# Performance work log

Measured on AMD Instinct MI355X. Metric: run time of the kernel, lower is better.

The kernel has to match this reference:

```python
import jax, jax.numpy as jnp
import numpy as np

B, S, D, H = 4, 2048, 1024, 16
NEG = -1e10  # matches the module's -10000000000.0 additive mask


def setup_inputs() -> dict:
    key = jax.random.key(0)
    k1, k2, k3, k4, k5 = jax.random.split(key, 5)
    scale = 0.02
    return {
        "x": jax.random.normal(k1, (B, S, D), dtype=jnp.float32),
        "w_qkv": jax.random.normal(k2, (D, 3 * D), dtype=jnp.float32) * scale,
        "b_qkv": jax.random.normal(k3, (3 * D,), dtype=jnp.float32) * scale,
        "w_out": jax.random.normal(k4, (D, D), dtype=jnp.float32) * scale,
        "b_out": jax.random.normal(k5, (D,), dtype=jnp.float32) * scale,
    }


def reference(x, w_qkv, b_qkv, w_out, b_out):
    b, s, d = x.shape
    hd = d // H  # per-head dim
    qkv = x @ w_qkv + b_qkv  # [b,s,3d]
    qq, kk, vv = jnp.split(qkv, 3, axis=-1)
    # [b,h,s,hd]
    qq = qq.reshape(b, s, H, hd).transpose(0, 2, 1, 3)
    kk = kk.reshape(b, s, H, hd).transpose(0, 2, 1, 3)
    vv = vv.reshape(b, s, H, hd).transpose(0, 2, 1, 3)
    scale = 1.0 / float(hd) ** 0.5
    # additive causal mask: NEG above diagonal, 0 on/below (as in module)
    mask = (1.0 - jnp.tri(s, dtype=jnp.float32)) * NEG
    attn = jnp.einsum("bhqd,bhkd->bhqk", qq, kk) * scale + mask
    attn = jax.nn.softmax(attn, axis=-1)
    out = jnp.einsum("bhqk,bhkd->bhqd", attn, vv)  # [b,h,s,hd]
    out = out.transpose(0, 2, 1, 3).reshape(b, s, d)
    return out @ w_out + b_out
```

## Files before the change

### kernel.cpp

```cpp
#include <hip/hip_runtime.h>
#include <hip/hip_bf16.h>
#include <stdint.h>


#define B_   4
#define S_   2048
#define D_   1024
#define H_   16
#define HD_  64
#define MTOK (B_ * S_)
#define BK   32
#define QSCALE 0.18033688011112042f

typedef __attribute__((ext_vector_type(8))) short bfx8;
typedef __attribute__((ext_vector_type(4))) float fx4;

static __device__ __forceinline__ unsigned short f2bf(float f) {
    union { float f; uint32_t u; } v{f};
    uint32_t u = v.u;
    u += 0x7fffu + ((u >> 16) & 1u);
    return (unsigned short)(u >> 16);
}

static __device__ __forceinline__ uint32_t cvtpk(float lo, float hi) {
    uint32_t r;
    asm volatile("v_cvt_pk_bf16_f32 %0, %1, %2" : "=v"(r) : "v"(lo), "v"(hi));
    return r;
}

static __device__ __forceinline__ void gll16(const unsigned short* g, const unsigned short* l) {
    typedef const __attribute__((address_space(1))) void* gp_t;
    typedef __attribute__((address_space(3))) void* lp_t;
    __builtin_amdgcn_global_load_lds((gp_t)(uintptr_t)g, (lp_t)(uint32_t)(uintptr_t)l, 16, 0, 0);
}

__global__ void k_conv_x(const float* __restrict__ x, unsigned short* __restrict__ xb, int n8) {
    int i = blockIdx.x * blockDim.x + threadIdx.x;
    int stride = gridDim.x * blockDim.x;
    for (; i < n8; i += stride) {
        const float4* p = (const float4*)(x + (size_t)i * 8);
        float4 a = p[0], b = p[1];
        bfx8 o;
        o[0]=f2bf(a.x); o[1]=f2bf(a.y); o[2]=f2bf(a.z); o[3]=f2bf(a.w);
        o[4]=f2bf(b.x); o[5]=f2bf(b.y); o[6]=f2bf(b.z); o[7]=f2bf(b.w);
        *(bfx8*)(xb + (size_t)i * 8) = o;
    }
}

__global__ void k_transpose_bf(const float* __restrict__ w, unsigned short* __restrict__ wt,
                               int K, int N) {
    int idx = blockIdx.x * blockDim.x + threadIdx.x;
    int total = N * (K / 8);
    if (idx >= total) return;
    int n  = idx % N;
    int k0 = (idx / N) * 8;
    bfx8 o;
#pragma unroll
    for (int j = 0; j < 8; ++j) o[j] = f2bf(w[(size_t)(k0 + j) * N + n]);
    *(bfx8*)(wt + (size_t)n * K + k0) = o;
}

__global__ void k_transpose_v(const unsigned short* __restrict__ Vw,
                              unsigned short* __restrict__ Vt) {
    __shared__ unsigned short lds[64][72];
    const int bg = blockIdx.x;
    const int bh = bg >> 5;
    const int st = (bg & 31) * 64;
    const int t = threadIdx.x;
#pragma unroll
    for (int j = 0; j < 2; ++j) {
        int c = t + 256 * j;
        int row = c >> 3, q = c & 7;
        *(bfx8*)&lds[row][q * 8] = *(const bfx8*)&Vw[((size_t)bh * S_ + st + row) * HD_ + q * 8];
    }
    __syncthreads();
#pragma unroll
    for (int j = 0; j < 2; ++j) {
        int c = t + 256 * j;
        int d = c >> 3, q = c & 7;
        bfx8 o;
#pragma unroll
        for (int e = 0; e < 8; ++e) o[e] = lds[q * 8 + e][d];
        *(bfx8*)&Vt[((size_t)bh * HD_ + d) * S_ + st + q * 8] = o;
    }
}

__launch_bounds__(256)
__global__ void k_gemm_qkv(const unsigned short* __restrict__ A,
                           const unsigned short* __restrict__ Bt,
                           const float* __restrict__ bias,
                           unsigned short* __restrict__ Qw,
                           unsigned short* __restrict__ Kw,
                           unsigned short* __restrict__ Vw) {
    __shared__ unsigned short Al[128 * BK];
    __shared__ unsigned short Bl[128 * BK];
    const int wg = blockIdx.x;
    const int lin = (wg & 7) * 192 + (wg >> 3);
    const int ny = lin / 24, nx = lin - ny * 24;
    const int m0 = ny * 128;
    const int n0 = nx * 128;
    const int t = threadIdx.x;
    const int w = t >> 6, l = t & 63;
    const int wr = w >> 1, wc = w & 1;
    const int lr = l & 15, lg = l >> 4;
    const int srow = l >> 2;
    const int scol = (l & 3) * 8;
    fx4 acc[4][4] = {};

    for (int k0 = 0; k0 < D_; k0 += BK) {
        __syncthreads();
#pragma unroll
        for (int j = 0; j < 2; ++j) {
            int rb = j * 64 + w * 16;
            gll16(&A [(size_t)(m0 + rb + srow) * D_ + k0 + scol], &Al[rb * BK]);
            gll16(&Bt[(size_t)(n0 + rb + srow) * D_ + k0 + scol], &Bl[rb * BK]);
        }
        __syncthreads();
        bfx8 af[4], bf[4];
#pragma unroll
        for (int i = 0; i < 4; ++i) af[i] = *(const bfx8*)&Al[(wr * 64 + i * 16 + lr) * BK + lg * 8];
#pragma unroll
        for (int i = 0; i < 4; ++i) bf[i] = *(const bfx8*)&Bl[(wc * 64 + i * 16 + lr) * BK + lg * 8];
#pragma unroll
        for (int mi = 0; mi < 4; ++mi)
#pragma unroll
            for (int ni = 0; ni < 4; ++ni)
                acc[mi][ni] = __builtin_amdgcn_mfma_f32_16x16x32_bf16(bf[ni], af[mi], acc[mi][ni], 0, 0, 0);
    }

#pragma unroll
    for (int ni = 0; ni < 4; ++ni) {
        const int nn = n0 + wc * 64 + ni * 16 + lg * 4;
        const int mat = nn >> 10;
        const int h = (nn & 1023) >> 6, dd = nn & 63;
        const float4 bv = *(const float4*)&bias[nn];
        unsigned short* dst = (mat == 0) ? Qw : (mat == 1) ? Kw : Vw;
        const float sc = (mat == 0) ? QSCALE : 1.0f;
#pragma unroll
        for (int mi = 0; mi < 4; ++mi) {
            const int m = m0 + wr * 64 + mi * 16 + lr;
            const int b = m >> 11, s = m & 2047;
            const int bh = b * H_ + h;
            fx4 v = acc[mi][ni];
            float o0 = (v[0] + bv.x) * sc, o1 = (v[1] + bv.y) * sc;
            float o2 = (v[2] + bv.z) * sc, o3 = (v[3] + bv.w) * sc;
            uint2 u; u.x = cvtpk(o0, o1); u.y = cvtpk(o2, o3);
            *(uint2*)&dst[((size_t)bh * S_ + s) * HD_ + dd] = u;
        }
    }
}

__launch_bounds__(512, 4)
__global__ void k_attn(const unsigned short* __restrict__ Qw,
                       const unsigned short* __restrict__ Kw,
                       const unsigned short* __restrict__ Vt,
                       unsigned short* __restrict__ Ob) {
    __shared__ unsigned short Kl[2][64 * 64];
    __shared__ unsigned short Vl[2][64 * 64];
    __shared__ unsigned short Pl[8][16 * 72];
    const int wg = blockIdx.x;
    const int xcd = wg & 7, ix = wg >> 3;
    const int bh = xcd * 8 + (ix >> 3);
    const int pi = ix & 7;
    const int t = threadIdx.x;
    const int w = t >> 6, l = t & 63;
    const int lr = l & 15, lg = l >> 4;
    const int qA = pi * 128 + w * 16;
    const int qB = (15 - pi) * 128 + w * 16;
    const int NT = 32 - 2 * pi;

    const unsigned short* Qp = Qw + (size_t)bh * S_ * HD_;
    const unsigned short* Kp = Kw + (size_t)bh * S_ * HD_;
    const unsigned short* Vp = Vt + (size_t)bh * HD_ * S_;

    bfx8 qfA[2], qfB[2];
#pragma unroll
    for (int kk = 0; kk < 2; ++kk) {
        qfA[kk] = *(const bfx8*)&Qp[(size_t)(qA + lr) * HD_ + kk * 32 + lg * 8];
        qfB[kk] = *(const bfx8*)&Qp[(size_t)(qB + lr) * HD_ + kk * 32 + lg * 8];
    }

    fx4 oA[4] = {}, oB[4] = {};
    float mA = -1e30f, lA = 0.f, mB = -1e30f, lB = 0.f;

    auto compute = [&](int qr, const bfx8* qf, fx4* oacc, float& mrow, float& lsum,
                       int kv0, int buf) {
        fx4 sacc[4] = {};
#pragma unroll
        for (int c = 0; c < 4; ++c) {
            int row = c * 16 + lr;
#pragma unroll
            for (int kk = 0; kk < 2; ++kk) {
                int colb = kk * 64 + lg * 16;
                bfx8 kf = *(const bfx8*)((const char*)&Kl[buf][0] + row * 128 + (colb ^ ((row & 7) << 4)));
                sacc[c] = __builtin_amdgcn_mfma_f32_16x16x32_bf16(kf, qf[kk], sacc[c], 0, 0, 0);
            }
        }
        if (kv0 + 63 > qr) {
            const int qrel = qr + lr - kv0;
#pragma unroll
            for (int c = 0; c < 4; ++c)
#pragma unroll
                for (int i = 0; i < 4; ++i)
                    if (c * 16 + lg * 4 + i > qrel) sacc[c][i] = -1e30f;
        }
        float mc0 = fmaxf(fmaxf(sacc[0][0], sacc[0][1]), fmaxf(sacc[0][2], sacc[0][3]));
        float mc1 = fmaxf(fmaxf(sacc[1][0], sacc[1][1]), fmaxf(sacc[1][2], sacc[1][3]));
        float mc2 = fmaxf(fmaxf(sacc[2][0], sacc[2][1]), fmaxf(sacc[2][2], sacc[2][3]));
        float mc3 = fmaxf(fmaxf(sacc[3][0], sacc[3][1]), fmaxf(sacc[3][2], sacc[3][3]));
        float mx = fmaxf(fmaxf(mc0, mc1), fmaxf(mc2, mc3));
        mx = fmaxf(mx, __shfl_xor(mx, 16));
        mx = fmaxf(mx, __shfl_xor(mx, 32));
        float mnew = fmaxf(mrow, mx);
        float al = exp2f(mrow - mnew);
        mrow = mnew;
        float ps = 0.f;
        uint32_t pk[4][2];
#pragma unroll
        for (int c = 0; c < 4; ++c)
#pragma unroll
            for (int r = 0; r < 2; ++r) {
                float p0 = exp2f(sacc[c][2 * r]     - mnew);
                float p1 = exp2f(sacc[c][2 * r + 1] - mnew);
                ps += p0 + p1;
                pk[c][r] = cvtpk(p0, p1);
            }
        ps += __shfl_xor(ps, 16);
        ps += __shfl_xor(ps, 32);
        lsum = lsum * al + ps;
#pragma unroll
        for (int c = 0; c < 4; ++c) {
            uint2 u; u.x = pk[c][0]; u.y = pk[c][1];
            *(uint2*)&Pl[w][lr * 72 + c * 16 + lg * 4] = u;
        }
#pragma unroll
        for (int c = 0; c < 4; ++c)
#pragma unroll
            for (int i = 0; i < 4; ++i) oacc[c][i] *= al;
#pragma unroll
        for (int kk = 0; kk < 2; ++kk) {
            bfx8 pf = *(const bfx8*)&Pl[w][lr * 72 + kk * 32 + lg * 8];
#pragma unroll
            for (int c = 0; c < 4; ++c) {
                int vrow = c * 16 + lr;
                int vcolb = kk * 64 + lg * 16;
                bfx8 vf = *(const bfx8*)((const char*)&Vl[buf][0] + vrow * 128 + (vcolb ^ ((vrow & 7) << 4)));
                oacc[c] = __builtin_amdgcn_mfma_f32_16x16x32_bf16(vf, pf, oacc[c], 0, 0, 0);
            }
        }
    };

    {
        bfx8 sreg[2];
#pragma unroll
        for (int it = 0; it < 2; ++it) {
            int id = t + 512 * it;
            int c = id & 511;
            int row = c >> 3, q = c & 7;
            if (id < 512) sreg[it] = *(const bfx8*)&Kp[(size_t)row * HD_ + q * 8];
            else          sreg[it] = *(const bfx8*)&Vp[(size_t)row * S_ + q * 8];
        }
#pragma unroll
        for (int it = 0; it < 2; ++it) {
            int id = t + 512 * it;
            int c = id & 511;
            int row = c >> 3, q = c & 7;
            int off = row * 128 + ((q * 16) ^ ((row & 7) << 4));
            char* base = (id < 512) ? (char*)&Kl[0][0] : (char*)&Vl[0][0];
            *(bfx8*)(base + off) = sreg[it];
        }
    }
    __syncthreads();

    int buf = 0;
    for (int tkv = 0; tkv < NT; ++tkv) {
        const int kv0 = tkv * 64;
        const bool pre = (tkv + 1 < NT);
        bfx8 sreg[2];
        if (pre) {
            const int kn = kv0 + 64;
#pragma unroll
            for (int it = 0; it < 2; ++it) {
                int id = t + 512 * it;
                int c = id & 511;
                int row = c >> 3, q = c & 7;
                if (id < 512) sreg[it] = *(const bfx8*)&Kp[(size_t)(kn + row) * HD_ + q * 8];
                else          sreg[it] = *(const bfx8*)&Vp[(size_t)row * S_ + kn + q * 8];
            }
        }
        if (kv0 <= qB + 15) compute(qB, qfB, oB, mB, lB, kv0, buf);
        if (kv0 <= qA + 15) compute(qA, qfA, oA, mA, lA, kv0, buf);
        if (pre) {
#pragma unroll
            for (int it = 0; it < 2; ++it) {
                int id = t + 512 * it;
                int c = id & 511;
                int row = c >> 3, q = c & 7;
                int off = row * 128 + ((q * 16) ^ ((row & 7) << 4));
                char* base = (id < 512) ? (char*)&Kl[buf ^ 1][0] : (char*)&Vl[buf ^ 1][0];
                *(bfx8*)(base + off) = sreg[it];
            }
        }
        __syncthreads();
        buf ^= 1;
    }

    const int b = bh >> 4, h = bh & 15;
    const float ivA = __builtin_amdgcn_rcpf(lA);
    const float ivB = __builtin_amdgcn_rcpf(lB);
#pragma unroll
    for (int c = 0; c < 4; ++c) {
        uint2 ua, ub;
        ua.x = cvtpk(oA[c][0] * ivA, oA[c][1] * ivA);
        ua.y = cvtpk(oA[c][2] * ivA, oA[c][3] * ivA);
        ub.x = cvtpk(oB[c][0] * ivB, oB[c][1] * ivB);
        ub.y = cvtpk(oB[c][2] * ivB, oB[c][3] * ivB);
        int col = h * 64 + c * 16 + lg * 4;
        *(uint2*)&Ob[((size_t)b * S_ + qA + lr) * D_ + col] = ua;
        *(uint2*)&Ob[((size_t)b * S_ + qB + lr) * D_ + col] = ub;
    }
}

__launch_bounds__(256)
__global__ void k_gemm_proj(const unsigned short* __restrict__ A,
                            const unsigned short* __restrict__ Bt,
                            const float* __restrict__ bias,
                            float* __restrict__ out) {
    __shared__ unsigned short Al[128 * BK];
    __shared__ unsigned short Bl[128 * BK];
    const int wg = blockIdx.x;
    const int lin = (wg & 7) * 64 + (wg >> 3);
    const int ny = lin >> 3, nx = lin & 7;
    const int m0 = ny * 128;
    const int n0 = nx * 128;
    const int t = threadIdx.x;
    const int w = t >> 6, l = t & 63;
    const int wr = w >> 1, wc = w & 1;
    const int lr = l & 15, lg = l >> 4;
    const int srow = l >> 2;
    const int scol = (l & 3) * 8;
    fx4 acc[4][4] = {};

    for (int k0 = 0; k0 < D_; k0 += BK) {
        __syncthreads();
#pragma unroll
        for (int j = 0; j < 2; ++j) {
            int rb = j * 64 + w * 16;
            gll16(&A [(size_t)(m0 + rb + srow) * D_ + k0 + scol], &Al[rb * BK]);
            gll16(&Bt[(size_t)(n0 + rb + srow) * D_ + k0 + scol], &Bl[rb * BK]);
        }
        __syncthreads();
        bfx8 af[4], bf[4];
#pragma unroll
        for (int i = 0; i < 4; ++i) af[i] = *(const bfx8*)&Al[(wr * 64 + i * 16 + lr) * BK + lg * 8];
#pragma unroll
        for (int i = 0; i < 4; ++i) bf[i] = *(const bfx8*)&Bl[(wc * 64 + i * 16 + lr) * BK + lg * 8];
#pragma unroll
        for (int mi = 0; mi < 4; ++mi)
#pragma unroll
            for (int ni = 0; ni < 4; ++ni)
                acc[mi][ni] = __builtin_amdgcn_mfma_f32_16x16x32_bf16(bf[ni], af[mi], acc[mi][ni], 0, 0, 0);
    }
#pragma unroll
    for (int ni = 0; ni < 4; ++ni) {
        const int nn = n0 + wc * 64 + ni * 16 + lg * 4;
        const float4 bv = *(const float4*)&bias[nn];
#pragma unroll
        for (int mi = 0; mi < 4; ++mi) {
            const int m = m0 + wr * 64 + mi * 16 + lr;
            fx4 v = acc[mi][ni];
            float4 o; o.x = v[0] + bv.x; o.y = v[1] + bv.y; o.z = v[2] + bv.z; o.w = v[3] + bv.w;
            *(float4*)&out[(size_t)m * D_ + nn] = o;
        }
    }
}

extern "C" void kernel_launch(void* const* d_in, const int* in_sizes, int n_in,
                              void* d_out, int out_size, void* d_ws, size_t ws_size,
                              hipStream_t stream) {
    const float* x     = (const float*)d_in[0];
    const float* w_qkv = (const float*)d_in[1];
    const float* b_qkv = (const float*)d_in[2];
    const float* w_out = (const float*)d_in[3];
    const float* b_out = (const float*)d_in[4];
    float* out = (float*)d_out;

    unsigned short* xb    = (unsigned short*)d_ws;
    unsigned short* wqkvT = xb    + (size_t)MTOK * D_;
    unsigned short* woutT = wqkvT + (size_t)3 * D_ * D_;
    unsigned short* Qw    = woutT + (size_t)D_ * D_;
    unsigned short* Kw    = Qw    + (size_t)MTOK * D_;
    unsigned short* Vw    = Kw    + (size_t)MTOK * D_;
    unsigned short* attnb = Vw    + (size_t)MTOK * D_;
    unsigned short* Vt    = xb;

    k_conv_x<<<2048, 256, 0, stream>>>(x, xb, MTOK * D_ / 8);
    k_transpose_bf<<<(3 * D_ * (D_ / 8)) / 256, 256, 0, stream>>>(w_qkv, wqkvT, D_, 3 * D_);
    k_transpose_bf<<<(D_ * (D_ / 8)) / 256, 256, 0, stream>>>(w_out, woutT, D_, D_);
    k_gemm_qkv<<<1536, 256, 0, stream>>>(xb, wqkvT, b_qkv, Qw, Kw, Vw);
    k_transpose_v<<<2048, 256, 0, stream>>>(Vw, Vt);
    k_attn<<<512, 512, 0, stream>>>(Qw, Kw, Vt, attnb);
    k_gemm_proj<<<512, 256, 0, stream>>>(attnb, woutT, b_out, out);
}
```

Before: 213.1 us.

## Lazy softmax rescale, MFMA row-sum, swizzled P buffer, and MFMA priority hints

The attention inner loop now rescales the running output and max only when some row's new max exceeds the old one by more than a threshold, so most tiles skip the rescale. The per-row exp sum is no longer reduced with shuffles; an extra MFMA against a ones vector accumulates it. The P staging buffer switches from padding to an XOR swizzle, which shrinks shared memory. MFMA sections are wrapped in setprio hints. The gains come from fewer VALU and shuffle ops per tile, at the cost of one extra MFMA per k-chunk. The threshold bounds exp values up to 2^8, which risks reduced bf16 precision in P.

Result: faster. 206.9 us (-2.9%).

```diff
diff --git a/kernel.cpp b/kernel.cpp
--- a/kernel.cpp
+++ b/kernel.cpp
@@ -157,7 +157,7 @@
                        unsigned short* __restrict__ Ob) {
     __shared__ unsigned short Kl[2][64 * 64];
     __shared__ unsigned short Vl[2][64 * 64];
-    __shared__ unsigned short Pl[8][16 * 72];
+    __shared__ unsigned short Pl[8][16 * 64];
     const int wg = blockIdx.x;
     const int xcd = wg & 7, ix = wg >> 3;
     const int bh = xcd * 8 + (ix >> 3);
@@ -180,12 +180,18 @@
         qfB[kk] = *(const bfx8*)&Qp[(size_t)(qB + lr) * HD_ + kk * 32 + lg * 8];
     }
 
+    bfx8 ones;
+#pragma unroll
+    for (int j = 0; j < 8; ++j) ones[j] = (short)0x3F80;
+
     fx4 oA[4] = {}, oB[4] = {};
-    float mA = -1e30f, lA = 0.f, mB = -1e30f, lB = 0.f;
-
-    auto compute = [&](int qr, const bfx8* qf, fx4* oacc, float& mrow, float& lsum,
+    fx4 sA = {}, sB = {};
+    float mA = -1e30f, mB = -1e30f;
+
+    auto compute = [&](int qr, const bfx8* qf, fx4* oacc, fx4& osum, float& mrow,
                        int kv0, int buf) {
         fx4 sacc[4] = {};
+        __builtin_amdgcn_s_setprio(1);
 #pragma unroll
         for (int c = 0; c < 4; ++c) {
             int row = c * 16 + lr;
@@ -196,6 +202,7 @@
                 sacc[c] = __builtin_amdgcn_mfma_f32_16x16x32_bf16(kf, qf[kk], sacc[c], 0, 0, 0);
             }
         }
+        __builtin_amdgcn_s_setprio(0);
         if (kv0 + 63 > qr) {
             const int qrel = qr + lr - kv0;
 #pragma unroll
@@ -211,35 +218,30 @@
         float mx = fmaxf(fmaxf(mc0, mc1), fmaxf(mc2, mc3));
         mx = fmaxf(mx, __shfl_xor(mx, 16));
         mx = fmaxf(mx, __shfl_xor(mx, 32));
-        float mnew = fmaxf(mrow, mx);
-        float al = exp2f(mrow - mnew);
-        mrow = mnew;
-        float ps = 0.f;
-        uint32_t pk[4][2];
-#pragma unroll
-        for (int c = 0; c < 4; ++c)
-#pragma unroll
-            for (int r = 0; r < 2; ++r) {
-                float p0 = exp2f(sacc[c][2 * r]     - mnew);
-                float p1 = exp2f(sacc[c][2 * r + 1] - mnew);
-                ps += p0 + p1;
-                pk[c][r] = cvtpk(p0, p1);
-            }
-        ps += __shfl_xor(ps, 16);
-        ps += __shfl_xor(ps, 32);
-        lsum = lsum * al + ps;
+        if (!__all(mx <= mrow + 8.f)) {
+            float mnew = fmaxf(mrow, mx);
+            float al = exp2f(mrow - mnew);
+            mrow = mnew;
+#pragma unroll
+            for (int c = 0; c < 4; ++c)
+#pragma unroll
+                for (int i = 0; i < 4; ++i) oacc[c][i] *= al;
+            osum[0] *= al;
+        }
 #pragma unroll
         for (int c = 0; c < 4; ++c) {
-            uint2 u; u.x = pk[c][0]; u.y = pk[c][1];
-            *(uint2*)&Pl[w][lr * 72 + c * 16 + lg * 4] = u;
-        }
-#pragma unroll
-        for (int c = 0; c < 4; ++c)
-#pragma unroll
-            for (int i = 0; i < 4; ++i) oacc[c][i] *= al;
+            float p0 = exp2f(sacc[c][0] - mrow);
+            float p1 = exp2f(sacc[c][1] - mrow);
+            float p2 = exp2f(sacc[c][2] - mrow);
+            float p3 = exp2f(sacc[c][3] - mrow);
+            uint2 u; u.x = cvtpk(p0, p1); u.y = cvtpk(p2, p3);
+            *(uint2*)((char*)&Pl[w][0] + lr * 128 + ((c * 32 + lg * 8) ^ ((lr & 7) << 4))) = u;
+        }
+        __builtin_amdgcn_s_setprio(1);
 #pragma unroll
         for (int kk = 0; kk < 2; ++kk) {
-            bfx8 pf = *(const bfx8*)&Pl[w][lr * 72 + kk * 32 + lg * 8];
+            bfx8 pf = *(const bfx8*)((const char*)&Pl[w][0] + lr * 128 + ((kk * 64 + lg * 16) ^ ((lr & 7) << 4)));
+            osum = __builtin_amdgcn_mfma_f32_16x16x32_bf16(ones, pf, osum, 0, 0, 0);
 #pragma unroll
             for (int c = 0; c < 4; ++c) {
                 int vrow = c * 16 + lr;
@@ -248,6 +250,7 @@
                 oacc[c] = __builtin_amdgcn_mfma_f32_16x16x32_bf16(vf, pf, oacc[c], 0, 0, 0);
             }
         }
+        __builtin_amdgcn_s_setprio(0);
     };
 
     {
@@ -288,8 +291,8 @@
                 else          sreg[it] = *(const bfx8*)&Vp[(size_t)row * S_ + kn + q * 8];
             }
         }
-        if (kv0 <= qB + 15) compute(qB, qfB, oB, mB, lB, kv0, buf);
-        if (kv0 <= qA + 15) compute(qA, qfA, oA, mA, lA, kv0, buf);
+        if (kv0 <= qB + 15) compute(qB, qfB, oB, sB, mB, kv0, buf);
+        if (kv0 <= qA + 15) compute(qA, qfA, oA, sA, mA, kv0, buf);
         if (pre) {
 #pragma unroll
             for (int it = 0; it < 2; ++it) {
@@ -306,8 +309,8 @@
     }
 
     const int b = bh >> 4, h = bh & 15;
-    const float ivA = __builtin_amdgcn_rcpf(lA);
-    const float ivB = __builtin_amdgcn_rcpf(lB);
+    const float ivA = __builtin_amdgcn_rcpf(sA[0]);
+    const float ivB = __builtin_amdgcn_rcpf(sB[0]);
 #pragma unroll
     for (int c = 0; c < 4; ++c) {
         uint2 ua, ub;
```
